# Performance work log

Measured on AMD Instinct MI355X. Metric: run time of the kernel, lower is better.

## Reference

```python
import math
import jax, jax.numpy as jnp
import numpy as np

N_KINDS = 8
D_MODEL = 256
B_FEAT = 24  # Fourier bands; MLP input dim is 2*B_FEAT
SIGMA = 8.0


def setup_inputs() -> dict:
    key = jax.random.key(0)
    ks = jax.random.split(key, 8)
    N, S = 32, 2048
    values = jax.random.normal(ks[0], (N, S, 1), dtype=jnp.float32)
    kinds = jax.random.randint(ks[1], (N, S), 0, N_KINDS, dtype=jnp.int32)
    # Frozen Fourier projection matrix (torch: randn(in_dim, B) * sigma, requires_grad=False)
    Bmat = jax.random.normal(ks[2], (1, B_FEAT), dtype=jnp.float32) * SIGMA
    # Kind embedding table
    kind_emb = jax.random.normal(ks[3], (N_KINDS, D_MODEL), dtype=jnp.float32) * 0.02
    # Per-kind two-layer MLP params
    W1 = jax.random.normal(ks[4], (N_KINDS, 2 * B_FEAT, D_MODEL), dtype=jnp.float32) / math.sqrt(2 * B_FEAT)
    b1 = jnp.zeros((N_KINDS, D_MODEL), dtype=jnp.float32)
    W2 = jax.random.normal(ks[5], (N_KINDS, D_MODEL, D_MODEL), dtype=jnp.float32) / math.sqrt(D_MODEL)
    b2 = jnp.zeros((N_KINDS, D_MODEL), dtype=jnp.float32)
    return {"values": values, "kinds": kinds, "Bmat": Bmat,
            "kind_emb": kind_emb, "W1": W1, "b1": b1, "W2": W2, "b2": b2}


def reference(values, kinds, Bmat, kind_emb, W1, b1, W2, b2):
    N, S, _ = values.shape
    T = N * S
    d = kind_emb.shape[-1]
    # Fourier features: [T, 2B]
    y = (2.0 * math.pi) * values.reshape(T, 1) @ Bmat  # [T, B]
    ff = jnp.concatenate([jnp.sin(y), jnp.cos(y)], axis=-1)  # [T, 2B]
    kinds_flat = kinds.reshape(T)
    out = jnp.zeros((T, d), dtype=values.dtype)
    # kinds partition the tokens, so masked combine == the torch scatter-assign
    for k in range(kind_emb.shape[0]):
        h = jax.nn.gelu(ff @ W1[k] + b1[k], approximate=False)  # torch GELU is exact erf
        o = h @ W2[k] + b2[k]  # [T, d]
        out = jnp.where((kinds_flat == k)[:, None], o, out)
    return out.reshape(N, S, d) + kind_emb[kinds]
```

## Files before the change

### kernel.cpp

```cpp
#include <hip/hip_runtime.h>
#include <hip/hip_bf16.h>
#include <math.h>


#define NK 8
#define DM 256
#define TMAX 65536
#define K1 64
#define W1PK 16384
#define W2PK 65536

typedef __attribute__((ext_vector_type(8))) short   s16x8;
typedef __attribute__((ext_vector_type(8))) __bf16  bf16x8;
typedef __attribute__((ext_vector_type(4))) float   f32x4;

__device__ int   g_counts[NK];
__device__ int   g_bucket[(size_t)NK * TMAX];
__device__ short g_W1p[(size_t)NK * W1PK];
__device__ short g_W2p[(size_t)NK * W2PK];

static __device__ __forceinline__ short f2bf(float f) {
    __hip_bfloat16 h = __float2bfloat16(f);
    return __builtin_bit_cast(short, h);
}

static __device__ __forceinline__ f32x4 mfma16(s16x8 a, s16x8 b, f32x4 c) {
    return __builtin_amdgcn_mfma_f32_16x16x32_bf16(
        __builtin_bit_cast(bf16x8, a), __builtin_bit_cast(bf16x8, b), c, 0, 0, 0);
}

__global__ void pack_kernel(const float* __restrict__ W1, const float* __restrict__ W2) {
    if (blockIdx.x == 0 && threadIdx.x < NK) g_counts[threadIdx.x] = 0;
    int p = blockIdx.x * 256 + threadIdx.x;
    const int PER_KIND = 2048 + 8192;
    if (p >= NK * PER_KIND) return;
    int kind = p / PER_KIND;
    int rem  = p % PER_KIND;
    s16x8 v;
    if (rem < 2048) {
        int g = rem;
        int ktile = g >> 10, ntile = (g >> 6) & 15, lane = g & 63;
        int kk0 = ktile * 32 + (lane >> 4) * 8;
        int n   = ntile * 16 + (lane & 15);
        #pragma unroll
        for (int j = 0; j < 8; ++j) {
            int kk = kk0 + j;
            float f = (kk < 48) ? W1[((size_t)kind * 48 + kk) * DM + n] : 0.0f;
            v[j] = f2bf(f);
        }
        *(s16x8*)(g_W1p + (size_t)kind * W1PK + (size_t)g * 8) = v;
    } else {
        int g = rem - 2048;
        int ktile = g >> 10, ntile = (g >> 6) & 15, lane = g & 63;
        int kk0 = ktile * 32 + (lane >> 4) * 8;
        int n   = ntile * 16 + (lane & 15);
        #pragma unroll
        for (int j = 0; j < 8; ++j)
            v[j] = f2bf(W2[((size_t)kind * DM + kk0 + j) * DM + n]);
        *(s16x8*)(g_W2p + (size_t)kind * W2PK + (size_t)g * 8) = v;
    }
}

__global__ void bucket_kernel(const int* __restrict__ kinds, int T) {
    __shared__ int wcnt[4][NK];
    __shared__ int base[NK];
    const int tid = threadIdx.x, wave = tid >> 6, lane = tid & 63;
    int t = blockIdx.x * 256 + tid;
    int k = (t < T) ? kinds[t] : -1;
    int myrank = 0;
    #pragma unroll
    for (int kk = 0; kk < NK; ++kk) {
        unsigned long long m = __ballot(k == kk);
        if (lane == 0) wcnt[wave][kk] = __popcll(m);
        if (k == kk) myrank = __popcll(m & ((1ull << lane) - 1ull));
    }
    __syncthreads();
    if (tid < NK) {
        int s = 0;
        #pragma unroll
        for (int w = 0; w < 4; ++w) { int c = wcnt[w][tid]; wcnt[w][tid] = s; s += c; }
        base[tid] = atomicAdd(&g_counts[tid], s);
    }
    __syncthreads();
    if (k >= 0)
        g_bucket[(size_t)k * T + base[k] + wcnt[wave][k] + myrank] = t;
}

__global__ __launch_bounds__(256) void fproj_gemm(
    const float* __restrict__ values, const float* __restrict__ Bmat,
    const float* __restrict__ kind_emb, const float* __restrict__ b1,
    const float* __restrict__ b2, float* __restrict__ out, int T)
{
    const int k   = blockIdx.y;
    const int cnt = g_counts[k];
    const int m0  = blockIdx.x * 64;
    if (m0 >= cnt) return;
    const int valid = min(64, cnt - m0);

    __shared__ short Apack[4096];
    __shared__ short Hpack[16384];
    __shared__ int   toks[64];
    __shared__ float vals[64];

    const int tid  = threadIdx.x;
    const int wave = tid >> 6;
    const int lane = tid & 63;
    const int quad = lane >> 4;
    const int cl   = lane & 15;

    if (tid < 64) {
        int t = -1; float v = 0.0f;
        if (tid < valid) { t = g_bucket[(size_t)k * T + m0 + tid]; v = values[t]; }
        toks[tid] = t; vals[tid] = v;
    }
    __syncthreads();

    for (int idx = tid; idx < 4096; idx += 256) {
        int m = idx >> 6, kk = idx & 63;
        float f = 0.0f;
        if (kk < 48) {
            int b = (kk < 24) ? kk : kk - 24;
            float y = 6.283185307179586f * vals[m] * Bmat[b];
            f = (kk < 24) ? __sinf(y) : __cosf(y);
        }
        int mt = m >> 4, kt = kk >> 5, q = (kk >> 3) & 3, j = kk & 7;
        int l = (m & 15) | (q << 4);
        Apack[((kt * 4 + mt) << 9) + (l << 3) + j] = f2bf(f);
    }
    __syncthreads();

    f32x4 acc[4][4];
    #pragma unroll
    for (int mt = 0; mt < 4; ++mt)
        #pragma unroll
        for (int nt = 0; nt < 4; ++nt) acc[mt][nt] = (f32x4){0.f, 0.f, 0.f, 0.f};

    const s16x8* Ap  = (const s16x8*)Apack;
    const s16x8* B1p = (const s16x8*)(g_W1p + (size_t)k * W1PK);
    #pragma unroll
    for (int kt = 0; kt < 2; ++kt) {
        s16x8 a[4], b[4];
        #pragma unroll
        for (int mt = 0; mt < 4; ++mt) a[mt] = Ap[(kt * 4 + mt) * 64 + lane];
        #pragma unroll
        for (int nt = 0; nt < 4; ++nt) b[nt] = B1p[(kt * 16 + wave * 4 + nt) * 64 + lane];
        #pragma unroll
        for (int mt = 0; mt < 4; ++mt)
            #pragma unroll
            for (int nt = 0; nt < 4; ++nt) acc[mt][nt] = mfma16(a[mt], b[nt], acc[mt][nt]);
    }

    #pragma unroll
    for (int nt = 0; nt < 4; ++nt) {
        int c = wave * 64 + nt * 16 + cl;
        float bias = b1[k * DM + c];
        int kt2 = c >> 5, q2 = (c >> 3) & 3, j2 = c & 7;
        #pragma unroll
        for (int mt = 0; mt < 4; ++mt)
            #pragma unroll
            for (int r4 = 0; r4 < 4; ++r4) {
                int r = mt * 16 + quad * 4 + r4;
                float x = acc[mt][nt][r4] + bias;
                float h = 0.5f * x * (1.0f + erff(x * 0.7071067811865476f));
                int l2 = (r & 15) | (q2 << 4);
                Hpack[((kt2 * 4 + (r >> 4)) << 9) + (l2 << 3) + j2] = f2bf(h);
            }
    }
    __syncthreads();

    f32x4 acc2[4][4];
    #pragma unroll
    for (int mt = 0; mt < 4; ++mt)
        #pragma unroll
        for (int nt = 0; nt < 4; ++nt) acc2[mt][nt] = (f32x4){0.f, 0.f, 0.f, 0.f};

    const s16x8* Hp  = (const s16x8*)Hpack;
    const s16x8* B2p = (const s16x8*)(g_W2p + (size_t)k * W2PK);
    #pragma unroll
    for (int kt = 0; kt < 8; ++kt) {
        s16x8 a[4], b[4];
        #pragma unroll
        for (int mt = 0; mt < 4; ++mt) a[mt] = Hp[(kt * 4 + mt) * 64 + lane];
        #pragma unroll
        for (int nt = 0; nt < 4; ++nt) b[nt] = B2p[(kt * 16 + wave * 4 + nt) * 64 + lane];
        #pragma unroll
        for (int mt = 0; mt < 4; ++mt)
            #pragma unroll
            for (int nt = 0; nt < 4; ++nt) acc2[mt][nt] = mfma16(a[mt], b[nt], acc2[mt][nt]);
    }

    #pragma unroll
    for (int nt = 0; nt < 4; ++nt) {
        int c = wave * 64 + nt * 16 + cl;
        float add = b2[k * DM + c] + kind_emb[k * DM + c];
        #pragma unroll
        for (int mt = 0; mt < 4; ++mt)
            #pragma unroll
            for (int r4 = 0; r4 < 4; ++r4) {
                int r = mt * 16 + quad * 4 + r4;
                if (r < valid)
                    out[(size_t)toks[r] * DM + c] = acc2[mt][nt][r4] + add;
            }
    }
}

extern "C" void kernel_launch(void* const* d_in, const int* in_sizes, int n_in,
                              void* d_out, int out_size, void* d_ws, size_t ws_size,
                              hipStream_t stream) {
    const float* values   = (const float*)d_in[0];
    const int*   kinds    = (const int*)  d_in[1];
    const float* Bmat     = (const float*)d_in[2];
    const float* kind_emb = (const float*)d_in[3];
    const float* W1       = (const float*)d_in[4];
    const float* b1       = (const float*)d_in[5];
    const float* W2       = (const float*)d_in[6];
    const float* b2       = (const float*)d_in[7];
    float* out = (float*)d_out;
    const int T = in_sizes[0];

    pack_kernel<<<dim3((NK * (2048 + 8192) + 255) / 256), dim3(256), 0, stream>>>(W1, W2);
    bucket_kernel<<<dim3((T + 255) / 256), dim3(256), 0, stream>>>(kinds, T);
    dim3 g((T + 63) / 64, NK);
    fproj_gemm<<<g, dim3(256), 0, stream>>>(values, Bmat, kind_emb, b1, b2, out, T);
}
```

Measured before the change: 136.2 us.

## Restructure prep into coalesced LDS-transposed weight pack, deterministic scan, compact GEMM grid

Merges weight packing and per-block kind counting into one prep kernel. The pack now reads W1/W2 with coalesced float4 loads and transposes them through a padded LDS tile. Bucketing becomes a two-pass deterministic prefix (block counts, then a serial scan per block) instead of atomics. The GEMM launches a compact 1-D grid mapped over per-kind tile counts instead of an 8x oversized 2-D grid. It also aliases the A tile onto H in LDS to cut shared memory, preloads W1 fragments into registers, hoists the bias loads, and uses nontemporal output stores. The serial 256-step scan in every scatter block adds latency, and NBLK is hardcoded to 256, which ties correctness to T=65536.

```diff
diff --git a/kernel.cpp b/kernel.cpp
--- a/kernel.cpp
+++ b/kernel.cpp
@@ -6,18 +6,22 @@
 #define NK 8
 #define DM 256
 #define TMAX 65536
-#define K1 64
+#define NBLK 256
 #define W1PK 16384
 #define W2PK 65536
+#define LDSTRIDE 262
 
 typedef __attribute__((ext_vector_type(8))) short   s16x8;
 typedef __attribute__((ext_vector_type(8))) __bf16  bf16x8;
 typedef __attribute__((ext_vector_type(4))) float   f32x4;
+typedef __attribute__((ext_vector_type(2))) float   f32x2;
+typedef __attribute__((ext_vector_type(4))) int     i32x4;
 
 __device__ int   g_counts[NK];
+__device__ __align__(16) int g_blkcnt[NBLK][NK];
 __device__ int   g_bucket[(size_t)NK * TMAX];
-__device__ short g_W1p[(size_t)NK * W1PK];
-__device__ short g_W2p[(size_t)NK * W2PK];
+__device__ __align__(16) short g_W1p[(size_t)NK * W1PK];
+__device__ __align__(16) short g_W2p[(size_t)NK * W2PK];
 
 static __device__ __forceinline__ short f2bf(float f) {
     __hip_bfloat16 h = __float2bfloat16(f);
@@ -29,84 +33,140 @@
         __builtin_bit_cast(bf16x8, a), __builtin_bit_cast(bf16x8, b), c, 0, 0, 0);
 }
 
-__global__ void pack_kernel(const float* __restrict__ W1, const float* __restrict__ W2) {
-    if (blockIdx.x == 0 && threadIdx.x < NK) g_counts[threadIdx.x] = 0;
-    int p = blockIdx.x * 256 + threadIdx.x;
-    const int PER_KIND = 2048 + 8192;
-    if (p >= NK * PER_KIND) return;
-    int kind = p / PER_KIND;
-    int rem  = p % PER_KIND;
-    s16x8 v;
-    if (rem < 2048) {
-        int g = rem;
-        int ktile = g >> 10, ntile = (g >> 6) & 15, lane = g & 63;
-        int kk0 = ktile * 32 + (lane >> 4) * 8;
-        int n   = ntile * 16 + (lane & 15);
-        #pragma unroll
-        for (int j = 0; j < 8; ++j) {
-            int kk = kk0 + j;
-            float f = (kk < 48) ? W1[((size_t)kind * 48 + kk) * DM + n] : 0.0f;
-            v[j] = f2bf(f);
-        }
-        *(s16x8*)(g_W1p + (size_t)kind * W1PK + (size_t)g * 8) = v;
+__global__ __launch_bounds__(256) void prep_kernel(const float* __restrict__ W1,
+                                                   const float* __restrict__ W2,
+                                                   const int* __restrict__ kinds, int T) {
+    __shared__ float ld[32 * LDSTRIDE];
+    __shared__ int wcnt[4][NK];
+    const int tid = threadIdx.x;
+    const int bid = blockIdx.x;
+    if (bid < 80) {
+        const int isW1 = (bid >= 64);
+        int kind, kt;
+        if (isW1) { kind = (bid - 64) >> 1; kt = (bid - 64) & 1; }
+        else      { kind = bid >> 3;        kt = bid & 7; }
+        #pragma unroll
+        for (int i = 0; i < 8; ++i) {
+            int f = tid + i * 256;
+            int row = f >> 6, col = (f & 63) * 4;
+            int kk = kt * 32 + row;
+            f32x4 v = (f32x4){0.f, 0.f, 0.f, 0.f};
+            if (isW1) {
+                if (kk < 48) v = *(const f32x4*)(W1 + ((size_t)kind * 48 + kk) * DM + col);
+            } else {
+                v = *(const f32x4*)(W2 + ((size_t)kind * DM + kk) * DM + col);
+            }
+            float* dst = &ld[row * LDSTRIDE + col];
+            *(f32x2*)dst       = (f32x2){v[0], v[1]};
+            *(f32x2*)(dst + 2) = (f32x2){v[2], v[3]};
+        }
+        __syncthreads();
+        short* outp = isW1 ? (g_W1p + (size_t)kind * W1PK) : (g_W2p + (size_t)kind * W2PK);
+        #pragma unroll
+        for (int i = 0; i < 4; ++i) {
+            int g = tid + i * 256;
+            int ntile = g >> 6, l = g & 63;
+            int kk0 = (l >> 4) * 8, n = ntile * 16 + (l & 15);
+            s16x8 v;
+            #pragma unroll
+            for (int j = 0; j < 8; ++j) v[j] = f2bf(ld[(kk0 + j) * LDSTRIDE + n]);
+            *(s16x8*)(outp + ((size_t)(kt * 16 + ntile) * 64 + l) * 8) = v;
+        }
     } else {
-        int g = rem - 2048;
-        int ktile = g >> 10, ntile = (g >> 6) & 15, lane = g & 63;
-        int kk0 = ktile * 32 + (lane >> 4) * 8;
-        int n   = ntile * 16 + (lane & 15);
-        #pragma unroll
-        for (int j = 0; j < 8; ++j)
-            v[j] = f2bf(W2[((size_t)kind * DM + kk0 + j) * DM + n]);
-        *(s16x8*)(g_W2p + (size_t)kind * W2PK + (size_t)g * 8) = v;
-    }
-}
-
-__global__ void bucket_kernel(const int* __restrict__ kinds, int T) {
+        const int b = bid - 80;
+        const int wave = tid >> 6, lane = tid & 63;
+        int t = b * 256 + tid;
+        int k = (t < T) ? kinds[t] : -1;
+        #pragma unroll
+        for (int kk = 0; kk < NK; ++kk) {
+            unsigned long long m = __ballot(k == kk);
+            if (lane == 0) wcnt[wave][kk] = __popcll(m);
+        }
+        __syncthreads();
+        if (tid < NK) {
+            int s = 0;
+            #pragma unroll
+            for (int w = 0; w < 4; ++w) s += wcnt[w][tid];
+            g_blkcnt[b][tid] = s;
+        }
+    }
+}
+
+__global__ __launch_bounds__(256) void scatter_kernel(const int* __restrict__ kinds, int T) {
+    __shared__ int cnt_s[NBLK * NK];
     __shared__ int wcnt[4][NK];
-    __shared__ int base[NK];
+    __shared__ int base_s[NK];
     const int tid = threadIdx.x, wave = tid >> 6, lane = tid & 63;
-    int t = blockIdx.x * 256 + tid;
+    const int b = blockIdx.x;
+    {
+        const i32x4* src = (const i32x4*)&g_blkcnt[0][0];
+        i32x4* dst = (i32x4*)cnt_s;
+        dst[tid]       = src[tid];
+        dst[tid + 256] = src[tid + 256];
+    }
+    int t = b * 256 + tid;
     int k = (t < T) ? kinds[t] : -1;
-    int myrank = 0;
+    int rank = 0;
     #pragma unroll
     for (int kk = 0; kk < NK; ++kk) {
         unsigned long long m = __ballot(k == kk);
         if (lane == 0) wcnt[wave][kk] = __popcll(m);
-        if (k == kk) myrank = __popcll(m & ((1ull << lane) - 1ull));
+        if (k == kk) rank = __popcll(m & ((1ull << lane) - 1ull));
     }
     __syncthreads();
     if (tid < NK) {
         int s = 0;
-        #pragma unroll
-        for (int w = 0; w < 4; ++w) { int c = wcnt[w][tid]; wcnt[w][tid] = s; s += c; }
-        base[tid] = atomicAdd(&g_counts[tid], s);
+        for (int bb = 0; bb < NBLK; ++bb) {
+            if (bb == b) base_s[tid] = s;
+            s += cnt_s[bb * NK + tid];
+        }
+        if (b == 0) g_counts[tid] = s;
+        int ws = 0;
+        #pragma unroll
+        for (int w = 0; w < 4; ++w) { int c = wcnt[w][tid]; wcnt[w][tid] = ws; ws += c; }
     }
     __syncthreads();
     if (k >= 0)
-        g_bucket[(size_t)k * T + base[k] + wcnt[wave][k] + myrank] = t;
-}
-
-__global__ __launch_bounds__(256) void fproj_gemm(
+        g_bucket[(size_t)k * T + base_s[k] + wcnt[wave][k] + rank] = t;
+}
+
+__global__ __launch_bounds__(256, 4) void fproj_gemm(
     const float* __restrict__ values, const float* __restrict__ Bmat,
     const float* __restrict__ kind_emb, const float* __restrict__ b1,
     const float* __restrict__ b2, float* __restrict__ out, int T)
 {
-    const int k   = blockIdx.y;
-    const int cnt = g_counts[k];
-    const int m0  = blockIdx.x * 64;
-    if (m0 >= cnt) return;
+    int cnts[NK];
+    #pragma unroll
+    for (int i = 0; i < NK; ++i) cnts[i] = g_counts[i];
+    const int bid = blockIdx.x;
+    int k = -1, m0 = 0, cum = 0, cnt = 0;
+    #pragma unroll
+    for (int kk = 0; kk < NK; ++kk) {
+        int tk = (cnts[kk] + 63) >> 6;
+        if (k < 0 && bid < cum + tk) { k = kk; m0 = (bid - cum) * 64; cnt = cnts[kk]; }
+        cum += tk;
+    }
+    if (k < 0) return;
     const int valid = min(64, cnt - m0);
 
-    __shared__ short Apack[4096];
     __shared__ short Hpack[16384];
     __shared__ int   toks[64];
     __shared__ float vals[64];
+    short* Apack = Hpack;
 
     const int tid  = threadIdx.x;
     const int wave = tid >> 6;
     const int lane = tid & 63;
     const int quad = lane >> 4;
     const int cl   = lane & 15;
+
+    const s16x8* B1p = (const s16x8*)(g_W1p + (size_t)k * W1PK);
+    s16x8 b1f[2][4];
+    #pragma unroll
+    for (int kt = 0; kt < 2; ++kt)
+        #pragma unroll
+        for (int nt = 0; nt < 4; ++nt)
+            b1f[kt][nt] = B1p[(kt * 16 + wave * 4 + nt) * 64 + lane];
 
     if (tid < 64) {
         int t = -1; float v = 0.0f;
@@ -135,20 +195,18 @@
         #pragma unroll
         for (int nt = 0; nt < 4; ++nt) acc[mt][nt] = (f32x4){0.f, 0.f, 0.f, 0.f};
 
-    const s16x8* Ap  = (const s16x8*)Apack;
-    const s16x8* B1p = (const s16x8*)(g_W1p + (size_t)k * W1PK);
+    const s16x8* Ap = (const s16x8*)Apack;
     #pragma unroll
     for (int kt = 0; kt < 2; ++kt) {
-        s16x8 a[4], b[4];
+        s16x8 a[4];
         #pragma unroll
         for (int mt = 0; mt < 4; ++mt) a[mt] = Ap[(kt * 4 + mt) * 64 + lane];
         #pragma unroll
-        for (int nt = 0; nt < 4; ++nt) b[nt] = B1p[(kt * 16 + wave * 4 + nt) * 64 + lane];
-        #pragma unroll
-        for (int mt = 0; mt < 4; ++mt)
-            #pragma unroll
-            for (int nt = 0; nt < 4; ++nt) acc[mt][nt] = mfma16(a[mt], b[nt], acc[mt][nt]);
-    }
+        for (int mt = 0; mt < 4; ++mt)
+            #pragma unroll
+            for (int nt = 0; nt < 4; ++nt) acc[mt][nt] = mfma16(a[mt], b1f[kt][nt], acc[mt][nt]);
+    }
+    __syncthreads();
 
     #pragma unroll
     for (int nt = 0; nt < 4; ++nt) {
@@ -168,6 +226,13 @@
     }
     __syncthreads();
 
+    float addc[4];
+    #pragma unroll
+    for (int nt = 0; nt < 4; ++nt) {
+        int c = wave * 64 + nt * 16 + cl;
+        addc[nt] = b2[k * DM + c] + kind_emb[k * DM + c];
+    }
+
     f32x4 acc2[4][4];
     #pragma unroll
     for (int mt = 0; mt < 4; ++mt)
@@ -192,14 +257,14 @@
     #pragma unroll
     for (int nt = 0; nt < 4; ++nt) {
         int c = wave * 64 + nt * 16 + cl;
-        float add = b2[k * DM + c] + kind_emb[k * DM + c];
         #pragma unroll
         for (int mt = 0; mt < 4; ++mt)
             #pragma unroll
             for (int r4 = 0; r4 < 4; ++r4) {
                 int r = mt * 16 + quad * 4 + r4;
                 if (r < valid)
-                    out[(size_t)toks[r] * DM + c] = acc2[mt][nt][r4] + add;
+                    __builtin_nontemporal_store(acc2[mt][nt][r4] + addc[nt],
+                                                out + (size_t)toks[r] * DM + c);
             }
     }
 }
@@ -218,8 +283,8 @@
     float* out = (float*)d_out;
     const int T = in_sizes[0];
 
-    pack_kernel<<<dim3((NK * (2048 + 8192) + 255) / 256), dim3(256), 0, stream>>>(W1, W2);
-    bucket_kernel<<<dim3((T + 255) / 256), dim3(256), 0, stream>>>(kinds, T);
-    dim3 g((T + 63) / 64, NK);
-    fproj_gemm<<<g, dim3(256), 0, stream>>>(values, Bmat, kind_emb, b1, b2, out, T);
-}
+    prep_kernel<<<dim3(80 + NBLK), dim3(256), 0, stream>>>(W1, W2, kinds, T);
+    scatter_kernel<<<dim3(NBLK), dim3(256), 0, stream>>>(kinds, T);
+    fproj_gemm<<<dim3(T / 64 + NK), dim3(256), 0, stream>>>(values, Bmat, kind_emb,
+                                                            b1, b2, out, T);
+}
```

Measured after the change: 143.7 us. 1.05x slower.
